# Optimization experiments

Hardware: AMD Instinct MI355X
Metric: run time of the kernel (lower is better)

The kernel has to match this reference:

```python
import jax, jax.numpy as jnp
import numpy as np

NUM_HEADS = 8
D_MODEL = 512
D_Q = D_MODEL // NUM_HEADS
B, S = 4, 2048


def setup_inputs() -> dict:
    key = jax.random.key(0)
    ks = jax.random.split(key, 7)
    bound = 1.0 / np.sqrt(D_MODEL)  # kaiming_uniform with a=sqrt(5) on fan_in=d_model
    return {
        "x_query": jax.random.normal(ks[0], (B, S, D_MODEL), dtype=jnp.float32),
        "x_key": jax.random.normal(ks[1], (B, S, D_MODEL), dtype=jnp.float32),
        "x_value": jax.random.normal(ks[2], (B, S, D_MODEL), dtype=jnp.float32),
        "Q": jax.random.uniform(ks[3], (NUM_HEADS, D_MODEL, D_Q), minval=-bound, maxval=bound, dtype=jnp.float32),
        "K": jax.random.uniform(ks[4], (NUM_HEADS, D_MODEL, D_Q), minval=-bound, maxval=bound, dtype=jnp.float32),
        "V": jax.random.uniform(ks[5], (NUM_HEADS, D_MODEL, D_Q), minval=-bound, maxval=bound, dtype=jnp.float32),
        "Wout": jax.random.uniform(ks[6], (D_MODEL, D_MODEL), minval=-bound, maxval=bound, dtype=jnp.float32),
    }


def reference(x_query, x_key, x_value, Q, K, V, Wout):
    # per-head projections: [B,S,d_model] x [H,d_model,d_q] -> [B,H,S,d_q]
    q = jnp.einsum('bsd,hdq->bhsq', x_query, Q)
    k = jnp.einsum('bsd,hdq->bhsq', x_key, K)
    v = jnp.einsum('bsd,hdq->bhsq', x_value, V)
    scale = 1.0 / jnp.sqrt(jnp.asarray(q.shape[-1], q.dtype))
    scores = jnp.einsum('bhsq,bhtq->bhst', q, k) * scale  # [B,H,S,S]
    attn = jax.nn.softmax(scores, axis=-1)
    heads = jnp.einsum('bhst,bhtq->bhsq', attn, v)  # [B,H,S,d_q]
    # faithful to original: .view(B, S, -1) on [B,H,S,d_q] layout (no transpose)
    concat = heads.reshape(heads.shape[0], heads.shape[2], -1)
    return concat @ Wout.T
```

## Files before the change

### kernel.cpp

```cpp
#include <hip/hip_runtime.h>
#include <math.h>

#define BATCH 4
#define SEQ   2048
#define DM    512
#define NH    8
#define DQ    64
#define BS    (BATCH*SEQ)
#define APAD  72

#define QSCALE 0.18033688011112042f

typedef short  short8   __attribute__((ext_vector_type(8)));
typedef float  floatx4  __attribute__((ext_vector_type(4)));
typedef float  floatx16 __attribute__((ext_vector_type(16)));
typedef unsigned short ushort8 __attribute__((ext_vector_type(8)));
typedef unsigned uintx2 __attribute__((ext_vector_type(2)));
typedef unsigned uintx4 __attribute__((ext_vector_type(4)));

__device__ __forceinline__ unsigned short f2bf(float f) {
    return (unsigned short)((__float_as_uint(f) + 0x8000u) >> 16);
}
__device__ __forceinline__ unsigned pack2bf(float a, float b) {
    unsigned ua = __float_as_uint(a) + 0x8000u;
    unsigned ub = __float_as_uint(b) + 0x8000u;
    return __builtin_amdgcn_perm(ub, ua, 0x07060302u);
}

__global__ __launch_bounds__(256) void convert_w_kernel(
    const float* __restrict__ Wq, const float* __restrict__ Wk,
    const float* __restrict__ Wv, const float* __restrict__ Wo,
    unsigned short* __restrict__ wt, unsigned short* __restrict__ wo)
{
    const int which = blockIdx.y;
    const int idx = blockIdx.x * 256 + threadIdx.x;
    if (which == 3) {
        float4 v = *(const float4*)(Wo + (size_t)idx * 4);
        uint2 o;
        o.x = pack2bf(v.x, v.y);
        o.y = pack2bf(v.z, v.w);
        *(uint2*)(wo + (size_t)idx * 4) = o;
    } else {
        const float* W = (which == 0) ? Wq : (which == 1) ? Wk : Wv;
        const int n   = idx & 511;
        const int dd0 = (idx >> 9) * 4;
        const int h = n >> 6, d = n & 63;
        uint2 o;
        o.x = pack2bf(W[((size_t)h * DM + dd0 + 0) * DQ + d],
                      W[((size_t)h * DM + dd0 + 1) * DQ + d]);
        o.y = pack2bf(W[((size_t)h * DM + dd0 + 2) * DQ + d],
                      W[((size_t)h * DM + dd0 + 3) * DQ + d]);
        *(uint2*)(wt + (size_t)which * (DM * DM) + (size_t)n * DM + dd0) = o;
    }
}

__global__ __launch_bounds__(256) void qkv_gemm_kernel(
    const float* __restrict__ Xq, const float* __restrict__ Xk,
    const float* __restrict__ Xv, const unsigned short* __restrict__ wt,
    unsigned short* __restrict__ Oq, unsigned short* __restrict__ Ok,
    unsigned short* __restrict__ Ovt)
{
    __shared__ unsigned short As[64][APAD];
    __shared__ unsigned short Bs[128][APAD];

    const int which = blockIdx.z;
    const float* X = (which == 0) ? Xq : (which == 1) ? Xk : Xv;
    const unsigned short* Bt = wt + (size_t)which * (DM * DM);

    const int m0 = blockIdx.x * 64;
    const int n0 = blockIdx.y * 128;
    const int t = threadIdx.x, w = t >> 6, lane = t & 63;
    const int quad = lane >> 4, qr = lane & 15;
    const int arow = t >> 4;
    const int acol = (t & 15) * 4;
    const int brow = t >> 3;
    const int bcol = (t & 7) * 8;
    const int mw = 32 * (w >> 1), nw = 64 * (w & 1);

    floatx4 acc[2][4] = {};
    float4  areg[4];
    ushort8 breg[4];

    #pragma unroll
    for (int i = 0; i < 4; ++i)
        areg[i] = *(const float4*)(X + (size_t)(m0 + i * 16 + arow) * DM + acol);
    #pragma unroll
    for (int i = 0; i < 4; ++i)
        breg[i] = *(const ushort8*)(Bt + (size_t)(n0 + i * 32 + brow) * DM + bcol);

    for (int k0 = 0; k0 < DM; k0 += 64) {
        __syncthreads();
        #pragma unroll
        for (int i = 0; i < 4; ++i) {
            uint2 o;
            o.x = pack2bf(areg[i].x, areg[i].y);
            o.y = pack2bf(areg[i].z, areg[i].w);
            *(uint2*)&As[i * 16 + arow][acol] = o;
        }
        #pragma unroll
        for (int i = 0; i < 4; ++i)
            *(ushort8*)&Bs[i * 32 + brow][bcol] = breg[i];
        __syncthreads();

        if (k0 + 64 < DM) {
            #pragma unroll
            for (int i = 0; i < 4; ++i)
                areg[i] = *(const float4*)(X + (size_t)(m0 + i * 16 + arow) * DM + k0 + 64 + acol);
            #pragma unroll
            for (int i = 0; i < 4; ++i)
                breg[i] = *(const ushort8*)(Bt + (size_t)(n0 + i * 32 + brow) * DM + k0 + 64 + bcol);
        }

        #pragma unroll
        for (int kh = 0; kh < 2; ++kh) {
            short8 af[2], bf[4];
            #pragma unroll
            for (int si = 0; si < 2; ++si)
                af[si] = *(const short8*)&As[mw + 16 * si + qr][kh * 32 + quad * 8];
            #pragma unroll
            for (int sj = 0; sj < 4; ++sj)
                bf[sj] = *(const short8*)&Bs[nw + 16 * sj + qr][kh * 32 + quad * 8];
            #pragma unroll
            for (int si = 0; si < 2; ++si)
                #pragma unroll
                for (int sj = 0; sj < 4; ++sj)
                    acc[si][sj] = __builtin_amdgcn_mfma_f32_16x16x32_bf16(
                        af[si], bf[sj], acc[si][sj], 0, 0, 0);
        }
    }

    if (which == 0) {
        #pragma unroll
        for (int si = 0; si < 2; ++si) {
            #pragma unroll
            for (int sj = 0; sj < 4; ++sj) {
                const int col = n0 + nw + 16 * sj + qr;
                const int h = col >> 6, d = col & 63;
                #pragma unroll
                for (int r = 0; r < 4; ++r) {
                    const int row = m0 + mw + 16 * si + quad * 4 + r;
                    const int b = row >> 11, s = row & (SEQ - 1);
                    Oq[((size_t)(b * NH + h) * SEQ + s) * DQ + d] = f2bf(acc[si][sj][r] * QSCALE);
                }
            }
        }
    } else if (which == 1) {
        #pragma unroll
        for (int si = 0; si < 2; ++si) {
            #pragma unroll
            for (int sj = 0; sj < 4; ++sj) {
                const int col = n0 + nw + 16 * sj + qr;
                const int h = col >> 6, d = col & 63;
                #pragma unroll
                for (int r = 0; r < 4; ++r) {
                    const int row = m0 + mw + 16 * si + quad * 4 + r;
                    const int b = row >> 11, s = row & (SEQ - 1);
                    Ok[(size_t)(b * NH + h) * (SEQ * DQ)
                       + (size_t)(((s >> 5) * 4 + (d >> 4)) << 9)
                       + ((((d >> 3) & 1) << 5) + (s & 31)) * 8 + (d & 7)] = f2bf(acc[si][sj][r]);
                }
            }
        }
    } else {
        #pragma unroll
        for (int si = 0; si < 2; ++si) {
            #pragma unroll
            for (int sj = 0; sj < 4; ++sj) {
                const int col = n0 + nw + 16 * sj + qr;
                const int h = col >> 6, d = col & 63;
                #pragma unroll
                for (int r = 0; r < 4; ++r) {
                    const int row = m0 + mw + 16 * si + quad * 4 + r;
                    const int b = row >> 11, s = row & (SEQ - 1);
                    Ovt[(size_t)(b * NH + h) * (SEQ * DQ)
                        + (size_t)((s >> 6) << 12) + (((s >> 5) & 1) << 11)
                        + ((d >> 5) << 10) + (((s >> 4) & 1) << 9)
                        + ((((s >> 3) & 1) << 5) + (d & 31)) * 8 + (s & 7)] = f2bf(acc[si][sj][r]);
                }
            }
        }
    }
}

__global__ __launch_bounds__(256) void out_gemm_kernel(
    const unsigned short* __restrict__ A, const unsigned short* __restrict__ Bt,
    float* __restrict__ C)
{
    __shared__ unsigned short As[64][APAD];
    __shared__ unsigned short Bs[64][APAD];

    const int m0 = blockIdx.x * 64;
    const int n0 = blockIdx.y * 64;
    const int t = threadIdx.x, w = t >> 6, lane = t & 63;
    const int quad = lane >> 4, qr = lane & 15;
    const int brow = t >> 3;
    const int bcol = (t & 7) * 8;
    const int mw = 32 * (w >> 1), nw = 32 * (w & 1);

    floatx4 acc[2][2] = {};
    ushort8 areg[2], breg[2];

    #pragma unroll
    for (int i = 0; i < 2; ++i) {
        areg[i] = *(const ushort8*)(A + (size_t)(m0 + i * 32 + brow) * DM + bcol);
        breg[i] = *(const ushort8*)(Bt + (size_t)(n0 + i * 32 + brow) * DM + bcol);
    }

    for (int k0 = 0; k0 < DM; k0 += 64) {
        __syncthreads();
        #pragma unroll
        for (int i = 0; i < 2; ++i) {
            *(ushort8*)&As[i * 32 + brow][bcol] = areg[i];
            *(ushort8*)&Bs[i * 32 + brow][bcol] = breg[i];
        }
        __syncthreads();

        if (k0 + 64 < DM) {
            #pragma unroll
            for (int i = 0; i < 2; ++i) {
                areg[i] = *(const ushort8*)(A + (size_t)(m0 + i * 32 + brow) * DM + k0 + 64 + bcol);
                breg[i] = *(const ushort8*)(Bt + (size_t)(n0 + i * 32 + brow) * DM + k0 + 64 + bcol);
            }
        }

        #pragma unroll
        for (int kh = 0; kh < 2; ++kh) {
            short8 af[2], bf[2];
            #pragma unroll
            for (int si = 0; si < 2; ++si)
                af[si] = *(const short8*)&As[mw + 16 * si + qr][kh * 32 + quad * 8];
            #pragma unroll
            for (int sj = 0; sj < 2; ++sj)
                bf[sj] = *(const short8*)&Bs[nw + 16 * sj + qr][kh * 32 + quad * 8];
            #pragma unroll
            for (int si = 0; si < 2; ++si)
                #pragma unroll
                for (int sj = 0; sj < 2; ++sj)
                    acc[si][sj] = __builtin_amdgcn_mfma_f32_16x16x32_bf16(
                        af[si], bf[sj], acc[si][sj], 0, 0, 0);
        }
    }

    #pragma unroll
    for (int si = 0; si < 2; ++si) {
        #pragma unroll
        for (int sj = 0; sj < 2; ++sj) {
            const int col = n0 + nw + 16 * sj + qr;
            #pragma unroll
            for (int r = 0; r < 4; ++r) {
                const int row = m0 + mw + 16 * si + quad * 4 + r;
                C[(size_t)row * DM + col] = acc[si][sj][r];
            }
        }
    }
}

__global__ __launch_bounds__(512, 2) void attn_kernel(
    const unsigned short* __restrict__ Qp, const unsigned short* __restrict__ Kf,
    const unsigned short* __restrict__ Vf, unsigned short* __restrict__ Hd)
{
    __shared__ float epi[128 * 66 + 256];

    const int f    = blockIdx.x;
    const int xcd  = f & 7;
    const int slot = f >> 3;
    const int tile = slot & 15;
    const int bhi  = (slot >> 4) * 8 + xcd;
    const int b = bhi >> 3, h = bhi & 7;

    const int s0 = tile * 128;
    const size_t bh   = (size_t)(b * NH + h);
    const size_t base = bh * SEQ * DQ;

    const int t    = threadIdx.x;
    const int w    = t >> 6;
    const int lane = t & 63;
    const int qh   = w >> 1;
    const int kh   = w & 1;
    const int ln31 = lane & 31;
    const int lh   = lane >> 5;

    short8 bq[4];
    {
        const unsigned short* gq = Qp + base + (size_t)(s0 + 32 * qh + ln31) * DQ + lh * 8;
        #pragma unroll
        for (int s = 0; s < 4; ++s)
            bq[s] = *(const short8*)(gq + 16 * s);
    }

    const unsigned short* pK = Kf + base + ((size_t)kh << 11) + (size_t)lane * 8;
    const unsigned short* pV = Vf + base + ((size_t)kh << 11) + (size_t)lane * 8;

    floatx16 accO[2] = {};
    float l_lane = 0.f;

    short8 ak[4], bv[4];
    #pragma unroll
    for (int s = 0; s < 4; ++s)
        ak[s] = *(const short8*)(pK + s * 512);
    #pragma unroll
    for (int a = 0; a < 2; ++a)
        #pragma unroll
        for (int s = 0; s < 2; ++s)
            bv[a * 2 + s] = *(const short8*)(pV + a * 1024 + s * 512);

    for (int kt = 0; kt < SEQ; kt += 64) {
        floatx16 z = {};
        __builtin_amdgcn_s_setprio(1);
        #pragma unroll
        for (int s = 0; s < 4; ++s)
            z = __builtin_amdgcn_mfma_f32_32x32x16_bf16(ak[s], bq[s], z, 0, 0, 0);
        __builtin_amdgcn_s_setprio(0);

        const int ktn = (kt + 64 < SEQ) ? kt + 64 : kt;
        {
            const unsigned short* nK = pK + ((size_t)(ktn >> 5) << 11);
            #pragma unroll
            for (int s = 0; s < 4; ++s)
                ak[s] = *(const short8*)(nK + s * 512);
        }

        unsigned wg[4][2];
        #pragma unroll
        for (int g = 0; g < 4; ++g) {
            const float p0 = __builtin_amdgcn_exp2f(z[4 * g + 0]);
            const float p1 = __builtin_amdgcn_exp2f(z[4 * g + 1]);
            const float p2 = __builtin_amdgcn_exp2f(z[4 * g + 2]);
            const float p3 = __builtin_amdgcn_exp2f(z[4 * g + 3]);
            l_lane += (p0 + p1) + (p2 + p3);
            wg[g][0] = pack2bf(p0, p1);
            wg[g][1] = pack2bf(p2, p3);
        }

        const uintx2 e0 = __builtin_amdgcn_permlane32_swap(wg[0][0], wg[1][0], false, false);
        const uintx2 e1 = __builtin_amdgcn_permlane32_swap(wg[0][1], wg[1][1], false, false);
        const uintx2 e2 = __builtin_amdgcn_permlane32_swap(wg[2][0], wg[3][0], false, false);
        const uintx2 e3 = __builtin_amdgcn_permlane32_swap(wg[2][1], wg[3][1], false, false);
        uintx4 ua0, ua1;
        ua0[0] = e0[0]; ua0[1] = e1[0]; ua0[2] = e0[1]; ua0[3] = e1[1];
        ua1[0] = e2[0]; ua1[1] = e3[0]; ua1[2] = e2[1]; ua1[3] = e3[1];
        const short8 ap0 = __builtin_bit_cast(short8, ua0);
        const short8 ap1 = __builtin_bit_cast(short8, ua1);

        __builtin_amdgcn_s_setprio(1);
        #pragma unroll
        for (int a = 0; a < 2; ++a) {
            accO[a] = __builtin_amdgcn_mfma_f32_32x32x16_bf16(ap0, bv[a * 2 + 0], accO[a], 0, 0, 0);
            accO[a] = __builtin_amdgcn_mfma_f32_32x32x16_bf16(ap1, bv[a * 2 + 1], accO[a], 0, 0, 0);
        }
        __builtin_amdgcn_s_setprio(0);

        {
            const unsigned short* nV = pV + ((size_t)(ktn >> 6) << 12);
            #pragma unroll
            for (int a = 0; a < 2; ++a)
                #pragma unroll
                for (int s = 0; s < 2; ++s)
                    bv[a * 2 + s] = *(const short8*)(nV + a * 1024 + s * 512);
        }
    }

    float l2 = l_lane + __shfl_xor(l_lane, 32);
    float* Obuf = epi;
    float* lbuf = epi + 128 * 66;

    if (kh == 0) {
        if (lane < 32) lbuf[qh * 32 + lane] = l2;
        #pragma unroll
        for (int a = 0; a < 2; ++a)
            #pragma unroll
            for (int r = 0; r < 16; ++r) {
                const int qrow = (r & 3) + 8 * (r >> 2) + 4 * lh;
                Obuf[(32 * qh + qrow) * 66 + 32 * a + ln31] = accO[a][r];
            }
    }
    __syncthreads();

    if (kh == 1) {
        const float ltot = l2 + lbuf[qh * 32 + ln31];
        if (lane < 32) lbuf[128 + qh * 32 + lane] = 1.0f / ltot;
        #pragma unroll
        for (int a = 0; a < 2; ++a)
            #pragma unroll
            for (int r = 0; r < 16; ++r) {
                const int qrow = (r & 3) + 8 * (r >> 2) + 4 * lh;
                const float o = accO[a][r] + Obuf[(32 * qh + qrow) * 66 + 32 * a + ln31];
                const float iv = lbuf[128 + qh * 32 + qrow];
                Hd[base + (size_t)(s0 + 32 * qh + qrow) * DQ + 32 * a + ln31] = f2bf(o * iv);
            }
    }
}

extern "C" void kernel_launch(void* const* d_in, const int* in_sizes, int n_in,
                              void* d_out, int out_size, void* d_ws, size_t ws_size,
                              hipStream_t stream) {
    const float* xq = (const float*)d_in[0];
    const float* xk = (const float*)d_in[1];
    const float* xv = (const float*)d_in[2];
    const float* Qw = (const float*)d_in[3];
    const float* Kw = (const float*)d_in[4];
    const float* Vw = (const float*)d_in[5];
    const float* Wo = (const float*)d_in[6];
    float* out = (float*)d_out;

    unsigned short* ws = (unsigned short*)d_ws;
    unsigned short* wt    = ws;
    unsigned short* wo    = ws + (size_t)786432;
    unsigned short* q_ws  = ws + (size_t)1048576;
    unsigned short* k_ws  = ws + (size_t)5242880;
    unsigned short* vt_ws = ws + (size_t)9437184;
    unsigned short* h_ws  = ws + (size_t)13631488;

    convert_w_kernel<<<dim3(256, 4), 256, 0, stream>>>(Qw, Kw, Vw, Wo, wt, wo);
    qkv_gemm_kernel<<<dim3(128, 4, 3), 256, 0, stream>>>(xq, xk, xv, wt, q_ws, k_ws, vt_ws);
    attn_kernel<<<dim3(512), 512, 0, stream>>>(q_ws, k_ws, vt_ws, h_ws);
    out_gemm_kernel<<<dim3(128, 8), 256, 0, stream>>>(h_ws, wo, out);
}
```

Before: 180.9 us.

## Compute softmax row sums via MFMA with ones vector and use hardware bf16 pack

Replaces the per-lane scalar accumulation of exponentials with two extra MFMA ops per tile that multiply the bf16 probability fragments by a ones vector, so row sums land directly in the output accumulator layout. It also swaps the manual round-and-permute bf16 packing for the v_cvt_pk_bf16_f32 instruction. The goal is to remove VALU adds and packing work from the softmax inner loop, at the cost of two more matrix ops per iteration and 16 extra accumulator registers. Row sums are now taken over the bf16-rounded probabilities, which matches what the PV product uses.

```diff
diff --git a/kernel.cpp b/kernel.cpp
--- a/kernel.cpp
+++ b/kernel.cpp
@@ -25,6 +25,11 @@
     unsigned ua = __float_as_uint(a) + 0x8000u;
     unsigned ub = __float_as_uint(b) + 0x8000u;
     return __builtin_amdgcn_perm(ub, ua, 0x07060302u);
+}
+__device__ __forceinline__ unsigned cvtpk(float a, float b) {
+    unsigned r;
+    asm("v_cvt_pk_bf16_f32 %0, %1, %2" : "=v"(r) : "v"(a), "v"(b));
+    return r;
 }
 
 __global__ __launch_bounds__(256) void convert_w_kernel(
@@ -259,7 +264,7 @@
     const unsigned short* __restrict__ Qp, const unsigned short* __restrict__ Kf,
     const unsigned short* __restrict__ Vf, unsigned short* __restrict__ Hd)
 {
-    __shared__ float epi[128 * 66 + 256];
+    __shared__ float epi[128 * 66 + 128];
 
     const int f    = blockIdx.x;
     const int xcd  = f & 7;
@@ -288,11 +293,15 @@
             bq[s] = *(const short8*)(gq + 16 * s);
     }
 
+    short8 vones;
+    #pragma unroll
+    for (int i = 0; i < 8; ++i) vones[i] = (short)0x3F80;
+
     const unsigned short* pK = Kf + base + ((size_t)kh << 11) + (size_t)lane * 8;
     const unsigned short* pV = Vf + base + ((size_t)kh << 11) + (size_t)lane * 8;
 
     floatx16 accO[2] = {};
-    float l_lane = 0.f;
+    floatx16 accL   = {};
 
     short8 ak[4], bv[4];
     #pragma unroll
@@ -327,9 +336,8 @@
             const float p1 = __builtin_amdgcn_exp2f(z[4 * g + 1]);
             const float p2 = __builtin_amdgcn_exp2f(z[4 * g + 2]);
             const float p3 = __builtin_amdgcn_exp2f(z[4 * g + 3]);
-            l_lane += (p0 + p1) + (p2 + p3);
-            wg[g][0] = pack2bf(p0, p1);
-            wg[g][1] = pack2bf(p2, p3);
+            wg[g][0] = cvtpk(p0, p1);
+            wg[g][1] = cvtpk(p2, p3);
         }
 
         const uintx2 e0 = __builtin_amdgcn_permlane32_swap(wg[0][0], wg[1][0], false, false);
@@ -348,6 +356,8 @@
             accO[a] = __builtin_amdgcn_mfma_f32_32x32x16_bf16(ap0, bv[a * 2 + 0], accO[a], 0, 0, 0);
             accO[a] = __builtin_amdgcn_mfma_f32_32x32x16_bf16(ap1, bv[a * 2 + 1], accO[a], 0, 0, 0);
         }
+        accL = __builtin_amdgcn_mfma_f32_32x32x16_bf16(ap0, vones, accL, 0, 0, 0);
+        accL = __builtin_amdgcn_mfma_f32_32x32x16_bf16(ap1, vones, accL, 0, 0, 0);
         __builtin_amdgcn_s_setprio(0);
 
         {
@@ -360,12 +370,17 @@
         }
     }
 
-    float l2 = l_lane + __shfl_xor(l_lane, 32);
     float* Obuf = epi;
     float* lbuf = epi + 128 * 66;
 
     if (kh == 0) {
-        if (lane < 32) lbuf[qh * 32 + lane] = l2;
+        if (ln31 == 0) {
+            #pragma unroll
+            for (int r = 0; r < 16; ++r) {
+                const int qrow = (r & 3) + 8 * (r >> 2) + 4 * lh;
+                lbuf[32 * qh + qrow] = accL[r];
+            }
+        }
         #pragma unroll
         for (int a = 0; a < 2; ++a)
             #pragma unroll
@@ -377,16 +392,19 @@
     __syncthreads();
 
     if (kh == 1) {
-        const float ltot = l2 + lbuf[qh * 32 + ln31];
-        if (lane < 32) lbuf[128 + qh * 32 + lane] = 1.0f / ltot;
+        float inv[16];
+        #pragma unroll
+        for (int r = 0; r < 16; ++r) {
+            const int qrow = (r & 3) + 8 * (r >> 2) + 4 * lh;
+            inv[r] = 1.0f / (accL[r] + lbuf[32 * qh + qrow]);
+        }
         #pragma unroll
         for (int a = 0; a < 2; ++a)
             #pragma unroll
             for (int r = 0; r < 16; ++r) {
                 const int qrow = (r & 3) + 8 * (r >> 2) + 4 * lh;
                 const float o = accO[a][r] + Obuf[(32 * qh + qrow) * 66 + 32 * a + ln31];
-                const float iv = lbuf[128 + qh * 32 + qrow];
-                Hd[base + (size_t)(s0 + 32 * qh + qrow) * DQ + 32 * a + ln31] = f2bf(o * iv);
+                Hd[base + (size_t)(s0 + 32 * qh + qrow) * DQ + 32 * a + ln31] = f2bf(o * inv[r]);
             }
     }
 }
```

New measurement: 180.5 us. Within noise of the previous version (-0.2%).
